# Performance work log

Hardware: AMD Instinct MI355X
Metric: run time of the kernel (lower is better)

## Reference

```python
import jax, jax.numpy as jnp
import numpy as np

N = 100000      # nodes
E = 1600000     # edges (avg degree 16)
F_IN = 64       # graph_input_dim
HID = 64        # gcn_out_dims (constant)
NG = 128        # number of graphs in batch
GF = 32         # global_input_dim
L1, L2, OUT = 256, 128, 1


def _glorot(k, fan_in, fan_out):
    s = 1.0 / np.sqrt(fan_in)
    return jax.random.uniform(k, (fan_in, fan_out), jnp.float32, -s, s)


def setup_inputs() -> dict:
    key = jax.random.key(0)
    ks = jax.random.split(key, 20)
    x = jax.random.normal(ks[0], (N, F_IN), jnp.float32)
    edge_index = jax.random.randint(ks[1], (2, E), 0, N, jnp.int64)
    # every graph gets a contiguous, non-empty slice of nodes (sorted batch ids)
    batch = (jnp.arange(N, dtype=jnp.int64) * NG) // N
    global_features = jax.random.normal(ks[2], (NG, GF), jnp.float32)
    dims = [F_IN, HID, HID, HID]
    inp = {"x": x, "global_features": global_features}
    for i in range(3):
        inp[f"conv_w{i+1}"] = _glorot(ks[3 + i], dims[i], dims[i + 1])
        inp[f"conv_b{i+1}"] = jnp.zeros((dims[i + 1],), jnp.float32)
    inp["fc_w1"] = _glorot(ks[8], HID * 2 + GF, L1)
    inp["fc_b1"] = jnp.zeros((L1,), jnp.float32)
    inp["fc_w2"] = _glorot(ks[9], L1, L2)
    inp["fc_b2"] = jnp.zeros((L2,), jnp.float32)
    inp["out_w"] = _glorot(ks[10], L2, OUT)
    inp["out_b"] = jnp.zeros((OUT,), jnp.float32)
    inp["edge_index"] = edge_index
    inp["batch"] = batch
    return inp


def _gcn_conv(x, src, dst, w, b, n):
    """PyG GCNConv: x' = D^-1/2 (A + I) D^-1/2 (x W) + b."""
    h = x @ w  # [n, out]
    loop = jnp.arange(n, dtype=src.dtype)
    s = jnp.concatenate([src, loop])
    d = jnp.concatenate([dst, loop])
    deg = jax.ops.segment_sum(jnp.ones(s.shape, h.dtype), d, num_segments=n)
    dinv = jnp.where(deg > 0, jax.lax.rsqrt(deg), 0.0)
    norm = dinv[s] * dinv[d]  # [E+n]
    out = jax.ops.segment_sum(h[s] * norm[:, None], d, num_segments=n)
    return out + b


def _forward(x, global_features, conv_w1, conv_b1, conv_w2, conv_b2,
             conv_w3, conv_b3, fc_w1, fc_b1, fc_w2, fc_b2, out_w, out_b,
             edge_index, batch):
    src, dst = edge_index[0], edge_index[1]
    n = x.shape[0]
    ng = global_features.shape[0]
    for w, b in ((conv_w1, conv_b1), (conv_w2, conv_b2), (conv_w3, conv_b3)):
        x = jax.nn.leaky_relu(_gcn_conv(x, src, dst, w, b, n))
    counts = jax.ops.segment_sum(jnp.ones((n,), x.dtype), batch, num_segments=ng)
    mean_pool = jax.ops.segment_sum(x, batch, num_segments=ng) / counts[:, None]
    max_pool = jax.ops.segment_max(x, batch, num_segments=ng)
    h = jnp.concatenate([mean_pool, max_pool, global_features], axis=1)
    h = jax.nn.leaky_relu(h @ fc_w1 + fc_b1)
    h = jax.nn.leaky_relu(h @ fc_w2 + fc_b2)
    return h @ out_w + out_b


def reference(x, global_features, conv_w1, conv_b1, conv_w2, conv_b2,
              conv_w3, conv_b3, fc_w1, fc_b1, fc_w2, fc_b2, out_w, out_b,
              edge_index, batch):
    return _forward(x, global_features, conv_w1, conv_b1, conv_w2, conv_b2,
                    conv_w3, conv_b3, fc_w1, fc_b1, fc_w2, fc_b2, out_w, out_b,
                    edge_index, batch)
```

## Files before the change

### kernel.cpp

```cpp
#include <hip/hip_runtime.h>
#include <hip/hip_fp16.h>
#include <stdint.h>

#define LRELU(x) ((x) > 0.0f ? (x) : 0.01f * (x))

struct h4 { __half2 a, b; };
struct h8 { __half2 a, b, c, d; };

typedef _Float16 f16x8 __attribute__((ext_vector_type(8)));
typedef float    f32x4 __attribute__((ext_vector_type(4)));

#define EPB 2048
#define PARTS 16


__global__ __launch_bounds__(256) void hist1_kernel(const int* __restrict__ dst,
                                                    int* __restrict__ bhist,
                                                    int nblk, int E, int nbk) {
    __shared__ int h[512];
    int blk = blockIdx.x, t = threadIdx.x;
    for (int i = t; i < nbk; i += 256) h[i] = 0;
    __syncthreads();
    #pragma unroll
    for (int k = 0; k < EPB / 1024; ++k) {
        int i4 = blk * (EPB / 4) + k * 256 + t;
        int e = i4 * 4;
        if (e + 3 < E) {
            int4 d = ((const int4*)dst)[i4];
            atomicAdd(&h[d.x >> 8], 1);
            atomicAdd(&h[d.y >> 8], 1);
            atomicAdd(&h[d.z >> 8], 1);
            atomicAdd(&h[d.w >> 8], 1);
        } else {
            for (int j = e; j < E; ++j) atomicAdd(&h[dst[j] >> 8], 1);
        }
    }
    __syncthreads();
    for (int i = t; i < nbk; i += 256) bhist[i * nblk + blk] = h[i];
}

__global__ __launch_bounds__(256) void scanb_kernel(int* __restrict__ bhist,
                                                    int* __restrict__ btot, int nblk) {
    __shared__ int s[256];
    __shared__ int carry;
    int b = blockIdx.x, t = threadIdx.x;
    if (t == 0) carry = 0;
    __syncthreads();
    for (int c0 = 0; c0 < nblk; c0 += 256) {
        int idx = c0 + t;
        int v = (idx < nblk) ? bhist[b * nblk + idx] : 0;
        s[t] = v;
        __syncthreads();
        for (int off = 1; off < 256; off <<= 1) {
            int a = (t >= off) ? s[t - off] : 0;
            __syncthreads();
            s[t] += a;
            __syncthreads();
        }
        if (idx < nblk) bhist[b * nblk + idx] = s[t] - v + carry;
        __syncthreads();
        if (t == 255) carry += s[255];
        __syncthreads();
    }
    if (t == 0) btot[b] = carry;
}

__global__ void bbase_kernel(const int* __restrict__ btot, int* __restrict__ bbase,
                             int nbk, int E) {
    __shared__ int s[512];
    int t = threadIdx.x;
    int v = (t < nbk) ? btot[t] : 0;
    s[t] = v;
    __syncthreads();
    for (int off = 1; off < 512; off <<= 1) {
        int a = (t >= off) ? s[t - off] : 0;
        __syncthreads();
        s[t] += a;
        __syncthreads();
    }
    if (t < nbk) bbase[t] = s[t] - v;
    if (t == 0) bbase[nbk] = E;
}

__global__ __launch_bounds__(256) void place_kernel(const int* __restrict__ src,
                                                    const int* __restrict__ dst,
                                                    const int* __restrict__ bbase,
                                                    const int* __restrict__ bhist,
                                                    unsigned* __restrict__ bedge,
                                                    int nblk, int E, int nbk) {
    __shared__ int cur[512];
    int blk = blockIdx.x, t = threadIdx.x;
    for (int i = t; i < nbk; i += 256) cur[i] = bbase[i] + bhist[i * nblk + blk];
    __syncthreads();
    #pragma unroll
    for (int k = 0; k < EPB / 1024; ++k) {
        int i4 = blk * (EPB / 4) + k * 256 + t;
        int e = i4 * 4;
        if (e + 3 < E) {
            int4 s4 = ((const int4*)src)[i4];
            int4 d4 = ((const int4*)dst)[i4];
            int p0 = atomicAdd(&cur[d4.x >> 8], 1);
            int p1 = atomicAdd(&cur[d4.y >> 8], 1);
            int p2 = atomicAdd(&cur[d4.z >> 8], 1);
            int p3 = atomicAdd(&cur[d4.w >> 8], 1);
            bedge[p0] = ((unsigned)s4.x << 8) | (unsigned)(d4.x & 255);
            bedge[p1] = ((unsigned)s4.y << 8) | (unsigned)(d4.y & 255);
            bedge[p2] = ((unsigned)s4.z << 8) | (unsigned)(d4.z & 255);
            bedge[p3] = ((unsigned)s4.w << 8) | (unsigned)(d4.w & 255);
        } else {
            for (int j = e; j < E; ++j) {
                int d = dst[j];
                int pos = atomicAdd(&cur[d >> 8], 1);
                bedge[pos] = ((unsigned)src[j] << 8) | (unsigned)(d & 255);
            }
        }
    }
}

__global__ __launch_bounds__(256) void csr_kernel(const unsigned* __restrict__ bedge,
                                                  const int* __restrict__ bbase,
                                                  int* __restrict__ row_ptr,
                                                  float* __restrict__ dinv,
                                                  int* __restrict__ csr_src,
                                                  int N, int E, int nbk) {
    __shared__ int cnt[256];
    __shared__ int s[256];
    __shared__ int cur[256];
    int b = blockIdx.x, t = threadIdx.x;
    int node0 = b << 8;
    int beg = bbase[b], end = bbase[b + 1];
    cnt[t] = 0;
    __syncthreads();
    for (int i = beg + t; i < end; i += 256) atomicAdd(&cnt[bedge[i] & 255u], 1);
    __syncthreads();
    int c = cnt[t];
    s[t] = c;
    __syncthreads();
    for (int off = 1; off < 256; off <<= 1) {
        int a = (t >= off) ? s[t - off] : 0;
        __syncthreads();
        s[t] += a;
        __syncthreads();
    }
    int rp = beg + s[t] - c;
    int node = node0 + t;
    if (node < N) {
        row_ptr[node] = rp;
        dinv[node] = rsqrtf((float)c + 1.0f);
    }
    cur[t] = rp;
    if (b == nbk - 1 && t == 0) row_ptr[N] = E;
    __syncthreads();
    for (int i = beg + t; i < end; i += 256) {
        unsigned u = bedge[i];
        int pos = atomicAdd(&cur[u & 255u], 1);
        csr_src[pos] = (int)(u >> 8);
    }
}


__global__ __launch_bounds__(256) void wprep_kernel(const float* __restrict__ w1,
                                                    const float* __restrict__ w2,
                                                    const float* __restrict__ w3,
                                                    _Float16* __restrict__ Bf) {
    int bc = blockIdx.x;
    int layer = bc >> 1, c = bc & 1;
    const float* W = (layer == 0) ? w1 : ((layer == 1) ? w2 : w3);
    int tid = threadIdx.x;
    int t = tid >> 6, l = tid & 63;
    _Float16* dst = Bf + ((size_t)(layer * 8 + c * 4 + t) * 64 + l) * 8;
    int n  = t * 16 + (l & 15);
    int kb = c * 32 + (l >> 4) * 8;
    #pragma unroll
    for (int i = 0; i < 8; ++i) dst[i] = (_Float16)W[(kb + i) * 64 + n];
}

template <bool XF32>
__global__ __launch_bounds__(256) void gemm_mfma_kernel(const void* __restrict__ Xv,
                                                        const _Float16* __restrict__ Bf,
                                                        const float* __restrict__ dinv,
                                                        __half* __restrict__ H, int N) {
    int w = threadIdx.x >> 6;
    int l = threadIdx.x & 63;
    int col = l & 15;
    int kg  = l >> 4;
    int base = blockIdx.x * 64 + w * 16;
    int nodeA = base + col;
    bool okA = nodeA < N;

    f32x4 acc[4] = {};
    #pragma unroll
    for (int c = 0; c < 2; ++c) {
        int k0 = c * 32 + kg * 8;
        f16x8 a = {};
        if (okA) {
            if constexpr (XF32) {
                const float* xp = (const float*)Xv + (size_t)nodeA * 64 + k0;
                float4 u = *(const float4*)xp;
                float4 v = *(const float4*)(xp + 4);
                a[0] = (_Float16)u.x; a[1] = (_Float16)u.y;
                a[2] = (_Float16)u.z; a[3] = (_Float16)u.w;
                a[4] = (_Float16)v.x; a[5] = (_Float16)v.y;
                a[6] = (_Float16)v.z; a[7] = (_Float16)v.w;
            } else {
                a = *(const f16x8*)((const __half*)Xv + (size_t)nodeA * 64 + k0);
            }
        }
        #pragma unroll
        for (int t = 0; t < 4; ++t) {
            f16x8 b = *(const f16x8*)(Bf + ((size_t)(c * 4 + t) * 64 + l) * 8);
            acc[t] = __builtin_amdgcn_mfma_f32_16x16x32_f16(a, b, acc[t], 0, 0, 0);
        }
    }
    float dvr[4];
    int rowN[4];
    #pragma unroll
    for (int r = 0; r < 4; ++r) {
        rowN[r] = base + kg * 4 + r;
        dvr[r] = (rowN[r] < N) ? dinv[rowN[r]] : 0.0f;
    }
    #pragma unroll
    for (int t = 0; t < 4; ++t) {
        #pragma unroll
        for (int r = 0; r < 4; ++r) {
            if (rowN[r] < N)
                H[(size_t)rowN[r] * 64 + t * 16 + col] = __float2half(acc[t][r] * dvr[r]);
        }
    }
}

#define ACC8(vv, c0, c1, c2, c3, c4, c5, c6, c7)                                \
    { float2 p;                                                                 \
      p = __half22float2((vv).a); c0 += p.x; c1 += p.y;                         \
      p = __half22float2((vv).b); c2 += p.x; c3 += p.y;                         \
      p = __half22float2((vv).c); c4 += p.x; c5 += p.y;                         \
      p = __half22float2((vv).d); c6 += p.x; c7 += p.y; }

__global__ __launch_bounds__(256) void agg_kernel(const __half* __restrict__ H,
                                                  const int* __restrict__ rp,
                                                  const int* __restrict__ csrc,
                                                  const float* __restrict__ dinv,
                                                  const float* __restrict__ bias,
                                                  __half* __restrict__ Y, int N) {
    int w = (blockIdx.x * blockDim.x + threadIdx.x) >> 6;
    int nA = w << 1;
    if (nA >= N) return;
    int nB = nA + 1;
    bool hasB = nB < N;
    int l = threadIdx.x & 63;
    int slot = l >> 3;
    int fo = (l & 7) << 3;
    int endA = rp[nA + 1];
    int eA = rp[nA] + slot;
    int endB = hasB ? rp[nB + 1] : 0;
    int eB = hasB ? (rp[nB] + slot) : 0;
    float a0=0,a1=0,a2=0,a3=0,a4=0,a5=0,a6=0,a7=0;
    float b0=0,b1=0,b2=0,b3=0,b4=0,b5=0,b6=0,b7=0;
    while (eA + 8 < endA && eB + 8 < endB) {
        int sA0 = csrc[eA], sA1 = csrc[eA + 8];
        int sB0 = csrc[eB], sB1 = csrc[eB + 8];
        h8 vA0 = *(const h8*)&H[(size_t)sA0 * 64 + fo];
        h8 vA1 = *(const h8*)&H[(size_t)sA1 * 64 + fo];
        h8 vB0 = *(const h8*)&H[(size_t)sB0 * 64 + fo];
        h8 vB1 = *(const h8*)&H[(size_t)sB1 * 64 + fo];
        ACC8(vA0, a0,a1,a2,a3,a4,a5,a6,a7);
        ACC8(vA1, a0,a1,a2,a3,a4,a5,a6,a7);
        ACC8(vB0, b0,b1,b2,b3,b4,b5,b6,b7);
        ACC8(vB1, b0,b1,b2,b3,b4,b5,b6,b7);
        eA += 16; eB += 16;
    }
    while (eA + 8 < endA) {
        int s0 = csrc[eA], s1 = csrc[eA + 8];
        h8 v0 = *(const h8*)&H[(size_t)s0 * 64 + fo];
        h8 v1 = *(const h8*)&H[(size_t)s1 * 64 + fo];
        ACC8(v0, a0,a1,a2,a3,a4,a5,a6,a7);
        ACC8(v1, a0,a1,a2,a3,a4,a5,a6,a7);
        eA += 16;
    }
    while (eB + 8 < endB) {
        int s0 = csrc[eB], s1 = csrc[eB + 8];
        h8 v0 = *(const h8*)&H[(size_t)s0 * 64 + fo];
        h8 v1 = *(const h8*)&H[(size_t)s1 * 64 + fo];
        ACC8(v0, b0,b1,b2,b3,b4,b5,b6,b7);
        ACC8(v1, b0,b1,b2,b3,b4,b5,b6,b7);
        eB += 16;
    }
    if (eA < endA) {
        h8 v0 = *(const h8*)&H[(size_t)csrc[eA] * 64 + fo];
        ACC8(v0, a0,a1,a2,a3,a4,a5,a6,a7);
    }
    if (eB < endB) {
        h8 v0 = *(const h8*)&H[(size_t)csrc[eB] * 64 + fo];
        ACC8(v0, b0,b1,b2,b3,b4,b5,b6,b7);
    }
    #pragma unroll
    for (int m = 8; m <= 32; m <<= 1) {
        a0 += __shfl_xor(a0, m); a1 += __shfl_xor(a1, m);
        a2 += __shfl_xor(a2, m); a3 += __shfl_xor(a3, m);
        a4 += __shfl_xor(a4, m); a5 += __shfl_xor(a5, m);
        a6 += __shfl_xor(a6, m); a7 += __shfl_xor(a7, m);
        b0 += __shfl_xor(b0, m); b1 += __shfl_xor(b1, m);
        b2 += __shfl_xor(b2, m); b3 += __shfl_xor(b3, m);
        b4 += __shfl_xor(b4, m); b5 += __shfl_xor(b5, m);
        b6 += __shfl_xor(b6, m); b7 += __shfl_xor(b7, m);
    }
    if (l < 8) {
        float4 bv0 = *(const float4*)&bias[fo];
        float4 bv1 = *(const float4*)&bias[fo + 4];
        {
            h8 hs = *(const h8*)&H[(size_t)nA * 64 + fo];
            float2 s0 = __half22float2(hs.a), s1 = __half22float2(hs.b);
            float2 s2 = __half22float2(hs.c), s3 = __half22float2(hs.d);
            float dv = dinv[nA];
            float o0 = LRELU(dv * (a0 + s0.x) + bv0.x);
            float o1 = LRELU(dv * (a1 + s0.y) + bv0.y);
            float o2 = LRELU(dv * (a2 + s1.x) + bv0.z);
            float o3 = LRELU(dv * (a3 + s1.y) + bv0.w);
            float o4 = LRELU(dv * (a4 + s2.x) + bv1.x);
            float o5 = LRELU(dv * (a5 + s2.y) + bv1.y);
            float o6 = LRELU(dv * (a6 + s3.x) + bv1.z);
            float o7 = LRELU(dv * (a7 + s3.y) + bv1.w);
            h8 o;
            o.a = __floats2half2_rn(o0, o1);
            o.b = __floats2half2_rn(o2, o3);
            o.c = __floats2half2_rn(o4, o5);
            o.d = __floats2half2_rn(o6, o7);
            *(h8*)&Y[(size_t)nA * 64 + fo] = o;
        }
        if (hasB) {
            h8 hs = *(const h8*)&H[(size_t)nB * 64 + fo];
            float2 s0 = __half22float2(hs.a), s1 = __half22float2(hs.b);
            float2 s2 = __half22float2(hs.c), s3 = __half22float2(hs.d);
            float dv = dinv[nB];
            float o0 = LRELU(dv * (b0 + s0.x) + bv0.x);
            float o1 = LRELU(dv * (b1 + s0.y) + bv0.y);
            float o2 = LRELU(dv * (b2 + s1.x) + bv0.z);
            float o3 = LRELU(dv * (b3 + s1.y) + bv0.w);
            float o4 = LRELU(dv * (b4 + s2.x) + bv1.x);
            float o5 = LRELU(dv * (b5 + s2.y) + bv1.y);
            float o6 = LRELU(dv * (b6 + s3.x) + bv1.z);
            float o7 = LRELU(dv * (b7 + s3.y) + bv1.w);
            h8 o;
            o.a = __floats2half2_rn(o0, o1);
            o.b = __floats2half2_rn(o2, o3);
            o.c = __floats2half2_rn(o4, o5);
            o.d = __floats2half2_rn(o6, o7);
            *(h8*)&Y[(size_t)nB * 64 + fo] = o;
        }
    }
}


__global__ void bounds_kernel(const int* __restrict__ batch, int* __restrict__ gstart,
                              int N, int NG) {
    int i = blockIdx.x * blockDim.x + threadIdx.x;
    if (i >= N) return;
    int b = batch[i];
    if (i == 0) {
        gstart[b] = 0;
        gstart[NG] = N;
    } else if (batch[i - 1] != b) {
        gstart[b] = i;
    }
}

__global__ __launch_bounds__(256) void pool1_kernel(const __half* __restrict__ Y,
                                                    const int* __restrict__ gstart,
                                                    float* __restrict__ pbuf) {
    __shared__ float ssum[8][64];
    __shared__ float smax[8][64];
    int g = blockIdx.x / PARTS;
    int p = blockIdx.x % PARTS;
    int t = threadIdx.x;
    int f2 = (t & 31) * 2;
    int rg = t >> 5;
    int s = gstart[g], epos = gstart[g + 1];
    int len = epos - s;
    int lo = s + (int)((long long)len * p / PARTS);
    int hi = s + (int)((long long)len * (p + 1) / PARTS);
    float sx = 0.f, sy = 0.f, mx = -3.0e38f, my = -3.0e38f;
    for (int r = lo + rg; r < hi; r += 8) {
        __half2 v = *(const __half2*)&Y[(size_t)r * 64 + f2];
        float2 f = __half22float2(v);
        sx += f.x; sy += f.y;
        mx = fmaxf(mx, f.x); my = fmaxf(my, f.y);
    }
    ssum[rg][f2] = sx; ssum[rg][f2 + 1] = sy;
    smax[rg][f2] = mx; smax[rg][f2 + 1] = my;
    __syncthreads();
    if (t < 64) {
        float ts = 0.f, tm = -3.0e38f;
        #pragma unroll
        for (int r = 0; r < 8; ++r) {
            ts += ssum[r][t];
            tm = fmaxf(tm, smax[r][t]);
        }
        float* row = &pbuf[(size_t)(g * PARTS + p) * 128];
        row[t] = ts;
        row[64 + t] = tm;
    }
}

__global__ __launch_bounds__(256) void mlp_kernel(const float* __restrict__ pbuf,
                                                  const int* __restrict__ gstart,
                                                  const float* __restrict__ gfeat,
                                                  const float* __restrict__ w1,
                                                  const float* __restrict__ b1,
                                                  const float* __restrict__ w2,
                                                  const float* __restrict__ b2,
                                                  const float* __restrict__ w3,
                                                  const float* __restrict__ b3,
                                                  float* __restrict__ out, int NG) {
    __shared__ float hl[160];
    __shared__ float h1[256];
    __shared__ float red[128];
    int g = blockIdx.x, t = threadIdx.x;
    if (t < 64) {
        const float* base = &pbuf[(size_t)g * PARTS * 128];
        float ts = 0.f, tm = -3.0e38f;
        #pragma unroll
        for (int p = 0; p < PARTS; ++p) {
            ts += base[p * 128 + t];
            tm = fmaxf(tm, base[p * 128 + 64 + t]);
        }
        float cnt = (float)(gstart[g + 1] - gstart[g]);
        hl[t] = ts / cnt;
        hl[64 + t] = tm;
    } else if (t >= 128 && t < 160) {
        hl[t] = gfeat[g * 32 + (t - 128)];
    }
    __syncthreads();
    float a1 = b1[t];
    for (int k = 0; k < 160; ++k) a1 += hl[k] * w1[k * 256 + t];
    h1[t] = LRELU(a1);
    __syncthreads();
    if (t < 128) {
        float a2 = b2[t];
        for (int k = 0; k < 256; ++k) a2 += h1[k] * w2[k * 128 + t];
        red[t] = LRELU(a2) * w3[t];
    }
    __syncthreads();
    if (t == 0) {
        float a3 = b3[0];
        for (int k = 0; k < 128; ++k) a3 += red[k];
        out[g] = a3;
    }
}


extern "C" void kernel_launch(void* const* d_in, const int* in_sizes, int n_in,
                              void* d_out, int out_size, void* d_ws, size_t ws_size,
                              hipStream_t stream) {
    const float* x      = (const float*)d_in[0];
    const float* gfeat  = (const float*)d_in[1];
    const float* cw1    = (const float*)d_in[2];
    const float* cb1    = (const float*)d_in[3];
    const float* cw2    = (const float*)d_in[4];
    const float* cb2    = (const float*)d_in[5];
    const float* cw3    = (const float*)d_in[6];
    const float* cb3    = (const float*)d_in[7];
    const float* fw1    = (const float*)d_in[8];
    const float* fb1    = (const float*)d_in[9];
    const float* fw2    = (const float*)d_in[10];
    const float* fb2    = (const float*)d_in[11];
    const float* ow     = (const float*)d_in[12];
    const float* ob     = (const float*)d_in[13];
    const int*   eidx   = (const int*)d_in[14];
    const int*   batch  = (const int*)d_in[15];

    const int N    = in_sizes[0] / 64;
    const int E    = in_sizes[14] / 2;
    const int NG   = in_sizes[1] / 32;
    const int NBUK = (N + 255) >> 8;
    const int NBLK = (E + EPB - 1) / EPB;
    const int* src = eidx;
    const int* dst = eidx + E;

    char* wp = (char*)d_ws;
    auto carve = [&](size_t bytes) {
        void* p = (void*)wp;
        wp += (bytes + 255) & ~(size_t)255;
        return p;
    };
    float*     dinv    = (float*)    carve((size_t)N * 4);
    int*       row_ptr = (int*)      carve((size_t)(N + 1) * 4);
    int*       bhist   = (int*)      carve((size_t)NBUK * NBLK * 4);
    int*       btot    = (int*)      carve((size_t)NBUK * 4);
    int*       bbase   = (int*)      carve((size_t)(NBUK + 1) * 4);
    unsigned*  bedge   = (unsigned*) carve((size_t)E * 4);
    int*       csr_src = (int*)      carve((size_t)E * 4);
    __half*    hbuf    = (__half*)   carve((size_t)N * 64 * 2);
    __half*    ybuf    = (__half*)   carve((size_t)N * 64 * 2);
    int*       gstart  = (int*)      carve((size_t)(NG + 1) * 4);
    float*     pbuf    = (float*)    carve((size_t)NG * PARTS * 128 * 4);
    _Float16*  Bf      = (_Float16*) carve((size_t)3 * 4096 * 2);
    float*     outf    = (float*)d_out;

    const int nbN = (N + 255) / 256;

    hist1_kernel<<<NBLK, 256, 0, stream>>>(dst, bhist, NBLK, E, NBUK);
    scanb_kernel<<<NBUK, 256, 0, stream>>>(bhist, btot, NBLK);
    bbase_kernel<<<1, 512, 0, stream>>>(btot, bbase, NBUK, E);
    place_kernel<<<NBLK, 256, 0, stream>>>(src, dst, bbase, bhist, bedge, NBLK, E, NBUK);
    csr_kernel<<<NBUK, 256, 0, stream>>>(bedge, bbase, row_ptr, dinv, csr_src, N, E, NBUK);
    bounds_kernel<<<nbN, 256, 0, stream>>>(batch, gstart, N, NG);
    wprep_kernel<<<6, 256, 0, stream>>>(cw1, cw2, cw3, Bf);

    const int gemmB = (N + 63) / 64;
    const int aggB  = ((N + 1) / 2 + 3) / 4;

    gemm_mfma_kernel<true ><<<gemmB, 256, 0, stream>>>(x,    Bf,        dinv, hbuf, N);
    agg_kernel<<<aggB, 256, 0, stream>>>(hbuf, row_ptr, csr_src, dinv, cb1, ybuf, N);
    gemm_mfma_kernel<false><<<gemmB, 256, 0, stream>>>(ybuf, Bf + 4096, dinv, hbuf, N);
    agg_kernel<<<aggB, 256, 0, stream>>>(hbuf, row_ptr, csr_src, dinv, cb2, ybuf, N);
    gemm_mfma_kernel<false><<<gemmB, 256, 0, stream>>>(ybuf, Bf + 8192, dinv, hbuf, N);
    agg_kernel<<<aggB, 256, 0, stream>>>(hbuf, row_ptr, csr_src, dinv, cb3, ybuf, N);

    pool1_kernel<<<NG * PARTS, 256, 0, stream>>>(ybuf, gstart, pbuf);
    mlp_kernel<<<NG, 256, 0, stream>>>(pbuf, gstart, gfeat, fw1, fb1, fw2, fb2, ow, ob, outf, NG);
}
```

Measured before the change: 229.9 us.

## Fold small setup kernels into neighbors and enlarge edges-per-block in CSR build

```diff
diff --git a/kernel.cpp b/kernel.cpp
--- a/kernel.cpp
+++ b/kernel.cpp
@@ -10,7 +10,7 @@
 typedef _Float16 f16x8 __attribute__((ext_vector_type(8)));
 typedef float    f32x4 __attribute__((ext_vector_type(4)));
 
-#define EPB 2048
+#define EPB 8192
 #define PARTS 16
 
 
@@ -65,21 +65,41 @@
     if (t == 0) btot[b] = carry;
 }
 
-__global__ void bbase_kernel(const int* __restrict__ btot, int* __restrict__ bbase,
-                             int nbk, int E) {
-    __shared__ int s[512];
-    int t = threadIdx.x;
-    int v = (t < nbk) ? btot[t] : 0;
-    s[t] = v;
-    __syncthreads();
-    for (int off = 1; off < 512; off <<= 1) {
-        int a = (t >= off) ? s[t - off] : 0;
+__global__ __launch_bounds__(512) void bbase_wprep_kernel(const int* __restrict__ btot,
+                                                          int* __restrict__ bbase,
+                                                          int nbk, int E,
+                                                          const float* __restrict__ w1,
+                                                          const float* __restrict__ w2,
+                                                          const float* __restrict__ w3,
+                                                          _Float16* __restrict__ Bf) {
+    if (blockIdx.x == 0) {
+        __shared__ int s[512];
+        int t = threadIdx.x;
+        int v = (t < nbk) ? btot[t] : 0;
+        s[t] = v;
         __syncthreads();
-        s[t] += a;
-        __syncthreads();
-    }
-    if (t < nbk) bbase[t] = s[t] - v;
-    if (t == 0) bbase[nbk] = E;
+        for (int off = 1; off < 512; off <<= 1) {
+            int a = (t >= off) ? s[t - off] : 0;
+            __syncthreads();
+            s[t] += a;
+            __syncthreads();
+        }
+        if (t < nbk) bbase[t] = s[t] - v;
+        if (t == 0) bbase[nbk] = E;
+    } else {
+        int bc = blockIdx.x - 1;
+        int tid = threadIdx.x;
+        if (tid < 256) {
+            int layer = bc >> 1, c = bc & 1;
+            const float* W = (layer == 0) ? w1 : ((layer == 1) ? w2 : w3);
+            int t = tid >> 6, l = tid & 63;
+            _Float16* dstp = Bf + ((size_t)(layer * 8 + c * 4 + t) * 64 + l) * 8;
+            int n  = t * 16 + (l & 15);
+            int kb = c * 32 + (l >> 4) * 8;
+            #pragma unroll
+            for (int i = 0; i < 8; ++i) dstp[i] = (_Float16)W[(kb + i) * 64 + n];
+        }
+    }
 }
 
 __global__ __launch_bounds__(256) void place_kernel(const int* __restrict__ src,
@@ -122,7 +142,9 @@
                                                   int* __restrict__ row_ptr,
                                                   float* __restrict__ dinv,
                                                   int* __restrict__ csr_src,
-                                                  int N, int E, int nbk) {
+                                                  const int* __restrict__ batch,
+                                                  int* __restrict__ gstart,
+                                                  int N, int E, int nbk, int NG) {
     __shared__ int cnt[256];
     __shared__ int s[256];
     __shared__ int cur[256];
@@ -147,6 +169,13 @@
     if (node < N) {
         row_ptr[node] = rp;
         dinv[node] = rsqrtf((float)c + 1.0f);
+        int bb = batch[node];
+        if (node == 0) {
+            gstart[bb] = 0;
+            gstart[NG] = N;
+        } else if (batch[node - 1] != bb) {
+            gstart[bb] = node;
+        }
     }
     cur[t] = rp;
     if (b == nbk - 1 && t == 0) row_ptr[N] = E;
@@ -158,22 +187,6 @@
     }
 }
 
-
-__global__ __launch_bounds__(256) void wprep_kernel(const float* __restrict__ w1,
-                                                    const float* __restrict__ w2,
-                                                    const float* __restrict__ w3,
-                                                    _Float16* __restrict__ Bf) {
-    int bc = blockIdx.x;
-    int layer = bc >> 1, c = bc & 1;
-    const float* W = (layer == 0) ? w1 : ((layer == 1) ? w2 : w3);
-    int tid = threadIdx.x;
-    int t = tid >> 6, l = tid & 63;
-    _Float16* dst = Bf + ((size_t)(layer * 8 + c * 4 + t) * 64 + l) * 8;
-    int n  = t * 16 + (l & 15);
-    int kb = c * 32 + (l >> 4) * 8;
-    #pragma unroll
-    for (int i = 0; i < 8; ++i) dst[i] = (_Float16)W[(kb + i) * 64 + n];
-}
 
 template <bool XF32>
 __global__ __launch_bounds__(256) void gemm_mfma_kernel(const void* __restrict__ Xv,
@@ -351,19 +364,6 @@
 }
 
 
-__global__ void bounds_kernel(const int* __restrict__ batch, int* __restrict__ gstart,
-                              int N, int NG) {
-    int i = blockIdx.x * blockDim.x + threadIdx.x;
-    if (i >= N) return;
-    int b = batch[i];
-    if (i == 0) {
-        gstart[b] = 0;
-        gstart[NG] = N;
-    } else if (batch[i - 1] != b) {
-        gstart[b] = i;
-    }
-}
-
 __global__ __launch_bounds__(256) void pool1_kernel(const __half* __restrict__ Y,
                                                     const int* __restrict__ gstart,
                                                     float* __restrict__ pbuf) {
@@ -496,15 +496,12 @@
     _Float16*  Bf      = (_Float16*) carve((size_t)3 * 4096 * 2);
     float*     outf    = (float*)d_out;
 
-    const int nbN = (N + 255) / 256;
-
     hist1_kernel<<<NBLK, 256, 0, stream>>>(dst, bhist, NBLK, E, NBUK);
     scanb_kernel<<<NBUK, 256, 0, stream>>>(bhist, btot, NBLK);
-    bbase_kernel<<<1, 512, 0, stream>>>(btot, bbase, NBUK, E);
+    bbase_wprep_kernel<<<7, 512, 0, stream>>>(btot, bbase, NBUK, E, cw1, cw2, cw3, Bf);
     place_kernel<<<NBLK, 256, 0, stream>>>(src, dst, bbase, bhist, bedge, NBLK, E, NBUK);
-    csr_kernel<<<NBUK, 256, 0, stream>>>(bedge, bbase, row_ptr, dinv, csr_src, N, E, NBUK);
-    bounds_kernel<<<nbN, 256, 0, stream>>>(batch, gstart, N, NG);
-    wprep_kernel<<<6, 256, 0, stream>>>(cw1, cw2, cw3, Bf);
+    csr_kernel<<<NBUK, 256, 0, stream>>>(bedge, bbase, row_ptr, dinv, csr_src,
+                                         batch, gstart, N, E, NBUK, NG);
 
     const int gemmB = (N + 63) / 64;
     const int aggB  = ((N + 1) / 2 + 3) / 4;
```

Result: faster. 219.8 us (-4.4%).
